# Kernel tuning notes

Measured on AMD Instinct MI355X. Metric: run time of the kernel, lower is better.

The kernel has to match this reference:

```python
import jax, jax.numpy as jnp
import numpy as np

HIDDEN = 1024
FRAME = 171
B = 128
T = 256


def _uniform(key, shape, fan):
    bound = 1.0 / np.sqrt(fan)
    return jax.random.uniform(key, shape, jnp.float32, -bound, bound)


def setup_inputs() -> dict:
    key = jax.random.key(0)
    ks = jax.random.split(key, 16)
    H, C = HIDDEN, FRAME
    inp = {
        "seq": jax.random.normal(ks[0], (B, T, C), jnp.float32),
        # LSTMCell 1 (input C -> H); torch layout: weight_ih [4H, in], weight_hh [4H, H]
        "w_ih1": _uniform(ks[1], (4 * H, C), H),
        "w_hh1": _uniform(ks[2], (4 * H, H), H),
        "b_ih1": _uniform(ks[3], (4 * H,), H),
        "b_hh1": _uniform(ks[4], (4 * H,), H),
        # LSTMCell 2 (H -> H)
        "w_ih2": _uniform(ks[5], (4 * H, H), H),
        "w_hh2": _uniform(ks[6], (4 * H, H), H),
        "b_ih2": _uniform(ks[7], (4 * H,), H),
        "b_hh2": _uniform(ks[8], (4 * H,), H),
        # LSTMCell 3 (H -> H)
        "w_ih3": _uniform(ks[9], (4 * H, H), H),
        "w_hh3": _uniform(ks[10], (4 * H, H), H),
        "b_ih3": _uniform(ks[11], (4 * H,), H),
        "b_hh3": _uniform(ks[12], (4 * H,), H),
        # Linear decoder H -> C
        "dec_w": _uniform(ks[13], (C, H), H),
        "dec_b": _uniform(ks[14], (C,), H),
        "gt": 5,
        "cond": 5,
    }
    return inp


def _lstm_cell(x, h, c, w_ih, w_hh, b_ih, b_hh):
    # torch.nn.LSTMCell: gates ordered (i, f, g, o)
    z = x @ w_ih.T + h @ w_hh.T + (b_ih + b_hh)  # [B, 4H]
    i, f, g, o = jnp.split(z, 4, axis=-1)
    c_new = jax.nn.sigmoid(f) * c + jax.nn.sigmoid(i) * jnp.tanh(g)
    h_new = jax.nn.sigmoid(o) * jnp.tanh(c_new)
    return h_new, c_new


def reference(seq, w_ih1, w_hh1, b_ih1, b_hh1,
              w_ih2, w_hh2, b_ih2, b_hh2,
              w_ih3, w_hh3, b_ih3, b_hh3,
              dec_w, dec_b, gt, cond):
    b, t, c = seq.shape
    h = seq.dtype
    # auto-conditioning pattern: gt ground-truth frames then cond self-fed frames
    pattern = (jnp.arange(t) % (gt + cond)) < gt  # [T] bool
    H = w_hh1.shape[1]
    zeros_h = jnp.zeros((b, H), h)
    init = (zeros_h, zeros_h, zeros_h, zeros_h, zeros_h, zeros_h,
            jnp.zeros((b, c), h))

    def step(carry, xs):
        h1, c1, h2, c2, h3, c3, xo = carry
        x_t, p_t = xs
        inp = jnp.where(p_t, x_t, xo)
        h1, c1 = _lstm_cell(inp, h1, c1, w_ih1, w_hh1, b_ih1, b_hh1)
        h2, c2 = _lstm_cell(h1, h2, c2, w_ih2, w_hh2, b_ih2, b_hh2)
        h3, c3 = _lstm_cell(h2, h3, c3, w_ih3, w_hh3, b_ih3, b_hh3)
        out = h3 @ dec_w.T + dec_b  # [B, C]
        return (h1, c1, h2, c2, h3, c3, out), out

    seq_t = jnp.transpose(seq, (1, 0, 2))  # [T, B, C]
    _, outs = jax.lax.scan(step, init, (seq_t, pattern))
    return jnp.transpose(outs, (1, 0, 2))  # [B, T, C]
```

## Files before the change

### kernel.cpp

```cpp
#include <hip/hip_runtime.h>
#include <math.h>

#define TSTEPS 256
#define CDIM 171
#define XSTR 6400
#define SEQB (TSTEPS*CDIM)

#define ARR_OFF   0
#define GF_OFF    2048
#define REL_OFF   2560
#define XCNT_OFF  3072
#define GREG_OFF  3080
#define ARR2_OFF  4096
#define NFLAGS    8192

typedef short v8s __attribute__((ext_vector_type(8)));
typedef float v4f __attribute__((ext_vector_type(4)));

static __device__ __forceinline__ unsigned short f2bf(float f) {
  unsigned int u = __float_as_uint(f);
  u += 0x7fffu + ((u >> 16) & 1u);
  return (unsigned short)(u >> 16);
}
static __device__ __forceinline__ float bf2f(unsigned short h) {
  return __uint_as_float(((unsigned int)h) << 16);
}
static __device__ __forceinline__ float sigf(float x) { return 1.0f / (1.0f + expf(-x)); }

static __device__ __forceinline__ bool probe_bf16(const unsigned int* w) {
  int c = 0;
  #pragma unroll
  for (int i = 0; i < 8; ++i) {
    unsigned e = (w[i] >> 7) & 0xFFu;
    c += (e >= 90u && e <= 145u) ? 1 : 0;
  }
  return c == 8;
}
static __device__ __forceinline__ float getv(const void* p, bool bf, size_t i) {
  return bf ? bf2f(((const unsigned short*)p)[i]) : ((const float*)p)[i];
}

static __device__ __forceinline__ unsigned ld_agent(const unsigned* p) {
  return __hip_atomic_load(p, __ATOMIC_RELAXED, __HIP_MEMORY_SCOPE_AGENT);
}
static __device__ __forceinline__ void st_agent(unsigned* p, unsigned v) {
  __hip_atomic_store(p, v, __ATOMIC_RELAXED, __HIP_MEMORY_SCOPE_AGENT);
}
static __device__ __forceinline__ void st_agent_us(unsigned short* p, unsigned short v) {
  __hip_atomic_store(p, v, __ATOMIC_RELAXED, __HIP_MEMORY_SCOPE_AGENT);
}

__global__ __launch_bounds__(256) void init_kernel(
    const void* seq, const void* wih1, const void* whh1,
    const void* bih1, const void* bhh1,
    const void* wih2, const void* whh2, const void* bih2, const void* bhh2,
    const void* wih3, const void* whh3, const void* bih3, const void* bhh3,
    const void* decw,
    unsigned short* __restrict__ X, float* __restrict__ BS,
    unsigned* __restrict__ flags,
    unsigned short* __restrict__ WL1, unsigned short* __restrict__ WL2,
    unsigned short* __restrict__ WL3, unsigned short* __restrict__ WDEC,
    unsigned short* __restrict__ XR, unsigned short* __restrict__ XGT,
    const int* __restrict__ gtp, const int* __restrict__ condp)
{
  const int tid = blockIdx.x * 256 + threadIdx.x;
  const int NT = 2048 * 256;
  const bool bfm = probe_bf16((const unsigned int*)seq);
  int gt = gtp[0];
  const bool p0 = 0 < gt;

  for (int i = tid; i < 128 * XSTR; i += NT) {
    int b = i / XSTR, c = i - b * XSTR;
    unsigned short v = 0;
    if (c < CDIM && p0) v = f2bf(getv(seq, bfm, (size_t)b * SEQB + c));
    X[i] = v;
  }
  for (int i = tid; i < 8 * 128 * XSTR; i += NT) {
    int r = i % (128 * XSTR);
    int b = r / XSTR, c = r - b * XSTR;
    unsigned short v = 0;
    if (c < CDIM && p0) v = f2bf(getv(seq, bfm, (size_t)b * SEQB + c));
    XR[i] = v;
  }
  const void* bis[3] = {bih1, bih2, bih3};
  const void* bhs[3] = {bhh1, bhh2, bhh3};
  for (int i = tid; i < 3 * 4096; i += NT) {
    int l = i >> 12, n = i & 4095;
    BS[i] = getv(bis[l], bfm, n) + getv(bhs[l], bfm, n);
  }
  for (int i = tid; i < NFLAGS; i += NT) flags[i] = 0u;
  for (int i = tid; i < 4096 * 1280; i += NT) {
    int r = i / 1280, c = i - r * 1280;
    float v;
    if (c < CDIM)      v = getv(wih1, bfm, (size_t)r * CDIM + c);
    else if (c < 256)  v = 0.f;
    else               v = getv(whh1, bfm, (size_t)r * 1024 + (c - 256));
    WL1[i] = f2bf(v);
  }
  for (int i = tid; i < 4096 * 2048; i += NT) {
    int r = i >> 11, c = i & 2047;
    size_t o = (size_t)r * 1024 + (c & 1023);
    WL2[i] = f2bf((c < 1024) ? getv(wih2, bfm, o) : getv(whh2, bfm, o));
    WL3[i] = f2bf((c < 1024) ? getv(wih3, bfm, o) : getv(whh3, bfm, o));
  }
  for (int i = tid; i < 176 * 1024; i += NT) {
    int r = i >> 10, c = i & 1023;
    WDEC[i] = (r < CDIM) ? f2bf(getv(decw, bfm, (size_t)r * 1024 + c)) : (unsigned short)0;
  }
  if (XGT) {
    for (int i = tid; i < TSTEPS * 128 * 256; i += NT) {
      int t = i >> 15, b = (i >> 8) & 127, c = i & 255;
      unsigned short v = 0;
      if (c < CDIM) v = f2bf(getv(seq, bfm, (size_t)b * SEQB + (size_t)t * CDIM + c));
      XGT[i] = v;
    }
  }
}

static __device__ __forceinline__ void gbar_nf(
    unsigned* fl, unsigned xcd, unsigned rank, unsigned NX, unsigned amask,
    unsigned G, int wave, int lane, unsigned& budget)
{
  __syncthreads();
  if (threadIdx.x == 0) st_agent(fl + ARR_OFF + xcd * 256 + rank, G);
  if (wave == 0) {
    if (rank == 0) {
      const unsigned* ab = fl + ARR_OFF + xcd * 256;
      for (;;) {
        unsigned ok = 1u;
        #pragma unroll
        for (int k = 0; k < 4; ++k) {
          unsigned r = (unsigned)lane + 64u * k;
          if (r < NX) ok &= (ld_agent(ab + r) >= G) ? 1u : 0u;
        }
        if (__all((int)ok)) break;
        if (budget == 0) break;
        --budget; __builtin_amdgcn_s_sleep(1);
      }
      st_agent(fl + GF_OFF + xcd * 64, G);
      for (;;) {
        unsigned ok = 1u;
        if (lane < 8 && ((amask >> lane) & 1u))
          ok = (ld_agent(fl + GF_OFF + (unsigned)lane * 64) >= G) ? 1u : 0u;
        if (__all((int)ok)) break;
        if (budget == 0) break;
        --budget; __builtin_amdgcn_s_sleep(1);
      }
      st_agent(fl + REL_OFF + xcd * 64, G);
    } else {
      unsigned* rp = fl + REL_OFF + xcd * 64;
      for (;;) {
        unsigned v = ld_agent(rp);
        if (__all((int)(v >= G))) break;
        if (budget == 0) break;
        --budget; __builtin_amdgcn_s_sleep(1);
      }
    }
  }
  __syncthreads();
}

static __device__ __forceinline__ void xcopy(
    unsigned short* __restrict__ dst, const unsigned short* __restrict__ src,
    int hoff, unsigned rank, unsigned NX, int tid)
{
  if (NX == 32u) {
    const unsigned d0 = rank * 256u + (unsigned)tid;
    unsigned vv[8];
    #pragma unroll
    for (int k = 0; k < 8; ++k) {
      unsigned d = d0 + 8192u * k;
      size_t off = (size_t)(d >> 9) * XSTR + hoff + ((size_t)(d & 511u) << 1);
      vv[k] = ld_agent((const unsigned*)(src + off));
    }
    #pragma unroll
    for (int k = 0; k < 8; ++k) {
      unsigned d = d0 + 8192u * k;
      size_t off = (size_t)(d >> 9) * XSTR + hoff + ((size_t)(d & 511u) << 1);
      *(unsigned*)(dst + off) = vv[k];
    }
  } else {
    for (unsigned d = rank * 256u + (unsigned)tid; d < 65536u; d += NX * 256u) {
      size_t off = (size_t)(d >> 9) * XSTR + hoff + ((size_t)(d & 511u) << 1);
      *(unsigned*)(dst + off) = ld_agent((const unsigned*)(src + off));
    }
  }
}

static __device__ __forceinline__ void xbar(
    unsigned* fl, unsigned xcd, unsigned rank, unsigned NX,
    unsigned G, int wave, int lane, unsigned& budget)
{
  __syncthreads();
  if (threadIdx.x == 0) st_agent(fl + ARR2_OFF + xcd * 256 + rank, G);
  if (wave == 0) {
    const unsigned* ab = fl + ARR2_OFF + xcd * 256;
    for (;;) {
      unsigned ok = 1u;
      #pragma unroll
      for (int k = 0; k < 4; ++k) {
        unsigned r = (unsigned)lane + 64u * k;
        if (r < NX) ok &= (ld_agent(ab + r) >= G) ? 1u : 0u;
      }
      if (__all((int)ok)) break;
      if (budget == 0) break;
      --budget; __builtin_amdgcn_s_sleep(1);
    }
    asm volatile("buffer_inv" ::: "memory");
  }
  __syncthreads();
}

template<int NCH>
static __device__ __forceinline__ void mfma_phase(
    const v8s* wf, const unsigned short* __restrict__ Xb,
    int a0, int bnd, int a1, int kbase, v4f* acc)
{
  #pragma unroll
  for (int i = 0; i < 8; ++i) acc[i] = (v4f){0.f, 0.f, 0.f, 0.f};
  #pragma unroll
  for (int c = 0; c < NCH; ++c) {
    const int acol = kbase + 32 * c;
    const int xcol = (acol < bnd) ? (a0 + acol) : (a1 + acol - bnd);
    const unsigned short* ap = Xb + xcol;
    #pragma unroll
    for (int m = 0; m < 8; ++m) {
      v8s a = *(const v8s*)(ap + (size_t)(16 * m) * XSTR);
      acc[m] = __builtin_amdgcn_mfma_f32_16x16x32_bf16(a, wf[c], acc[m], 0, 0, 0);
    }
  }
}

static __device__ __forceinline__ void lstm_epilogue(
    v4f* acc, float* lred, int wave, int lane,
    const float* bs4, float* cst2,
    unsigned short* __restrict__ X, int hoff, int g)
{
  const int l15 = lane & 15, quad = lane >> 4;
  float* myp = lred + wave * 2048;
  #pragma unroll
  for (int m = 0; m < 8; ++m)
    #pragma unroll
    for (int j = 0; j < 4; ++j)
      myp[m * 256 + l15 * 16 + ((4 * quad + j) ^ ((l15 >> 1) & 3))] = acc[m][j];
  __syncthreads();
  const int ri = lane >> 2, hc = lane & 3;
  #pragma unroll
  for (int e = 0; e < 2; ++e) {
    const int m = 2 * wave + e;
    float z[4];
    #pragma unroll
    for (int k = 0; k < 4; ++k) z[k] = bs4[k];
    #pragma unroll
    for (int w2 = 0; w2 < 4; ++w2) {
      const float* pp = lred + w2 * 2048 + m * 256;
      #pragma unroll
      for (int k = 0; k < 4; ++k) {
        const int col = hc + 4 * k;
        z[k] += pp[col * 16 + (ri ^ ((col >> 1) & 3))];
      }
    }
    float cn = sigf(z[1]) * cst2[e] + sigf(z[0]) * tanhf(z[2]);
    float h  = sigf(z[3]) * tanhf(cn);
    cst2[e] = cn;
    const int row = 32 * wave + 16 * e + ri;
    st_agent_us(X + (size_t)row * XSTR + hoff + 4 * g + hc, f2bf(h));
  }
}

static __device__ __forceinline__ void dec_tile(
    int dm2, int dn2, const unsigned short* __restrict__ WDEC,
    const unsigned short* __restrict__ XRb, int p_, float* lred,
    int wave, int lane, int l15, int quad,
    const void* __restrict__ decb, bool bf, bool wout, bool wx,
    void* __restrict__ outp, int t)
{
  v4f da = (v4f){0.f, 0.f, 0.f, 0.f};
  const unsigned short* wp = WDEC + (size_t)(16 * dn2 + l15) * 1024 + 256 * wave + 8 * quad;
  const unsigned short* ap = XRb + (size_t)(16 * dm2 + l15) * XSTR
                           + (4352 + 1024 * p_) + 256 * wave + 8 * quad;
  #pragma unroll
  for (int c = 0; c < 8; ++c) {
    v8s a = *(const v8s*)(ap + 32 * c);
    v8s w = *(const v8s*)(wp + 32 * c);
    da = __builtin_amdgcn_mfma_f32_16x16x32_bf16(a, w, da, 0, 0, 0);
  }
  float* myp = lred + wave * 2048;
  #pragma unroll
  for (int j = 0; j < 4; ++j)
    myp[l15 * 16 + ((4 * quad + j) ^ ((l15 >> 1) & 3))] = da[j];
  __syncthreads();
  if (wave == 0) {
    const int col = 16 * dn2 + l15;
    float dbv2 = (col < CDIM) ? getv(decb, bf, col) : 0.f;
    #pragma unroll
    for (int e = 0; e < 4; ++e) {
      const int r = 4 * e + quad;
      float v = dbv2;
      #pragma unroll
      for (int w2 = 0; w2 < 4; ++w2)
        v += lred[w2 * 2048 + l15 * 16 + (r ^ ((l15 >> 1) & 3))];
      if (col < CDIM) {
        const int brow = 16 * dm2 + r;
        if (wout) {
          const size_t oidx = (size_t)brow * SEQB + (size_t)t * CDIM + col;
          if (bf) ((unsigned short*)outp)[oidx] = f2bf(v);
          else    ((float*)outp)[oidx] = v;
        }
        if (wx) *(unsigned short*)((unsigned short*)XRb
                  + (size_t)brow * XSTR + col) = f2bf(v);
      }
    }
  }
  __syncthreads();
}

__global__ __launch_bounds__(256, 1) void persist(
    const unsigned short* __restrict__ WL1, const unsigned short* __restrict__ WL2,
    const unsigned short* __restrict__ WL3, const unsigned short* __restrict__ WDEC,
    const float* __restrict__ BS, unsigned short* __restrict__ X,
    unsigned* __restrict__ flags, unsigned short* __restrict__ XR,
    const void* __restrict__ seq, const void* __restrict__ decb,
    void* __restrict__ outp, const unsigned short* __restrict__ XGT,
    const int* __restrict__ gtp, const int* __restrict__ condp)
{
  const int g = blockIdx.x;
  const int tid = threadIdx.x, wave = tid >> 6, lane = tid & 63;
  const int l15 = lane & 15, quad = lane >> 4;
  const bool bf = probe_bf16((const unsigned int*)seq);
  int gt = gtp[0]; int per = gt + condp[0]; if (per < 1) per = 1;
  unsigned budget = 20000000u;

  __shared__ unsigned s_rank;
  unsigned xcd;
  asm volatile("s_getreg_b32 %0, hwreg(HW_REG_XCC_ID)" : "=s"(xcd));
  xcd &= 7u;
  if (tid == 0) {
    s_rank = __hip_atomic_fetch_add(flags + XCNT_OFF + xcd, 1u,
                                    __ATOMIC_RELAXED, __HIP_MEMORY_SCOPE_AGENT);
    __hip_atomic_fetch_add(flags + GREG_OFF, 1u,
                           __ATOMIC_RELEASE, __HIP_MEMORY_SCOPE_AGENT);
  }
  __syncthreads();
  const unsigned rank = s_rank;
  if (wave == 0 && lane == 0) {
    while (__hip_atomic_load(flags + GREG_OFF, __ATOMIC_ACQUIRE,
                             __HIP_MEMORY_SCOPE_AGENT) < 256u) {
      if (budget == 0) break;
      --budget; __builtin_amdgcn_s_sleep(4);
    }
  }
  __syncthreads();
  const unsigned NX = ld_agent(flags + XCNT_OFF + xcd);
  unsigned amask = 0;
  #pragma unroll
  for (int k = 0; k < 8; ++k)
    amask |= (ld_agent(flags + XCNT_OFF + k) > 0u ? 1u : 0u) << k;
  const unsigned owner = (unsigned)__builtin_ctz(amask | 0x100u);
  const bool isown = (xcd == owner);

  unsigned short* XRb = XR + (size_t)xcd * (128 * XSTR);

  const int br = 1024 * (l15 >> 2) + 4 * g + (l15 & 3);
  v8s w1f[10], w2f[16], w3f[16];
  {
    const unsigned short* p = WL1 + (size_t)br * 1280 + 320 * wave + 8 * quad;
    #pragma unroll
    for (int c = 0; c < 10; ++c) w1f[c] = *(const v8s*)(p + 32 * c);
  }
  {
    const unsigned short* p = WL2 + (size_t)br * 2048 + 512 * wave + 8 * quad;
    #pragma unroll
    for (int c = 0; c < 16; ++c) w2f[c] = *(const v8s*)(p + 32 * c);
  }
  {
    const unsigned short* p = WL3 + (size_t)br * 2048 + 512 * wave + 8 * quad;
    #pragma unroll
    for (int c = 0; c < 16; ++c) w3f[c] = *(const v8s*)(p + 32 * c);
  }
  const int dm = g / 11, dn = g - dm * 11;
  float bsr[3][4];
  #pragma unroll
  for (int l = 0; l < 3; ++l)
    #pragma unroll
    for (int gm = 0; gm < 4; ++gm)
      bsr[l][gm] = BS[4096 * l + 1024 * gm + 4 * g + (lane & 3)];

  float cst1[2] = {0.f, 0.f}, cst2v[2] = {0.f, 0.f}, cst3[2] = {0.f, 0.f};
  __shared__ float lred[8192];
  const unsigned short* Xb = XRb + (size_t)l15 * XSTR + 8 * quad;
  unsigned bgen = 0;
  v4f acc[8];

  for (int t = 0; t < TSTEPS; ++t) {
    const int p_ = t & 1, q_ = p_ ^ 1;
    const bool pt = (t % per) < gt;

    if (pt && wave == 0) {
      #pragma unroll
      for (int i = 0; i < 8; ++i) acc[i] = (v4f){0.f, 0.f, 0.f, 0.f};
      if (XGT) {
        const unsigned short* xb = XGT + ((size_t)t * 128 + l15) * 256 + 8 * quad;
        #pragma unroll
        for (int c = 0; c < 8; ++c) {
          #pragma unroll
          for (int m = 0; m < 8; ++m) {
            v8s a = *(const v8s*)(xb + 32 * c + (size_t)(16 * m) * 256);
            acc[m] = __builtin_amdgcn_mfma_f32_16x16x32_bf16(a, w1f[c], acc[m], 0, 0, 0);
          }
        }
      } else {
        #pragma unroll
        for (int c = 0; c < 8; ++c) {
          const int col0 = 32 * c + 8 * quad;
          #pragma unroll
          for (int m = 0; m < 8; ++m) {
            const size_t so = (size_t)(l15 + 16 * m) * SEQB + (size_t)t * CDIM;
            v8s a;
            #pragma unroll
            for (int j = 0; j < 8; ++j) {
              const int cc = col0 + j;
              unsigned short hv = 0;
              if (cc < CDIM)
                hv = bf ? ((const unsigned short*)seq)[so + cc]
                        : f2bf(((const float*)seq)[so + cc]);
              a[j] = (short)hv;
            }
            acc[m] = __builtin_amdgcn_mfma_f32_16x16x32_bf16(a, w1f[c], acc[m], 0, 0, 0);
          }
        }
      }
      #pragma unroll
      for (int c = 8; c < 10; ++c) {
        const unsigned short* ap = Xb + (256 + 1024 * q_) + (32 * c - 256);
        #pragma unroll
        for (int m = 0; m < 8; ++m) {
          v8s a = *(const v8s*)(ap + (size_t)(16 * m) * XSTR);
          acc[m] = __builtin_amdgcn_mfma_f32_16x16x32_bf16(a, w1f[c], acc[m], 0, 0, 0);
        }
      }
    } else {
      mfma_phase<10>(w1f, Xb, 0, 256, 256 + 1024 * q_, 320 * wave, acc);
    }
    lstm_epilogue(acc, lred, wave, lane, bsr[0], cst1, X, 256 + 1024 * p_, g);

    gbar_nf(flags, xcd, rank, NX, amask, ++bgen, wave, lane, budget);
    xcopy(XRb, X, 256 + 1024 * p_, rank, NX, tid);
    xbar(flags, xcd, rank, NX, bgen, wave, lane, budget);
    mfma_phase<16>(w2f, Xb, 256 + 1024 * p_, 1024, 2304 + 1024 * q_, 512 * wave, acc);
    lstm_epilogue(acc, lred, wave, lane, bsr[1], cst2v, X, 2304 + 1024 * p_, g);

    gbar_nf(flags, xcd, rank, NX, amask, ++bgen, wave, lane, budget);
    xcopy(XRb, X, 2304 + 1024 * p_, rank, NX, tid);
    xbar(flags, xcd, rank, NX, bgen, wave, lane, budget);
    mfma_phase<16>(w3f, Xb, 2304 + 1024 * p_, 1024, 4352 + 1024 * q_, 512 * wave, acc);
    lstm_epilogue(acc, lred, wave, lane, bsr[2], cst3, X, 4352 + 1024 * p_, g);

    gbar_nf(flags, xcd, rank, NX, amask, ++bgen, wave, lane, budget);
    xcopy(XRb, X, 4352 + 1024 * p_, rank, NX, tid);
    xbar(flags, xcd, rank, NX, bgen, wave, lane, budget);

    const bool pnext = ((t + 1) % per) < gt;
    const bool needx = (t < TSTEPS - 1) && !pnext;
    if (needx) {
      for (unsigned tt = rank; tt < 88u; tt += NX) {
        int dm2 = (int)(tt / 11u), dn2 = (int)(tt - (unsigned)dm2 * 11u);
        dec_tile(dm2, dn2, WDEC, XRb, p_, lred, wave, lane, l15, quad,
                 decb, bf, isown, true, outp, t);
      }
      ++bgen;
      xbar(flags, xcd, rank, NX, bgen, wave, lane, budget);
    } else if (g < 88) {
      dec_tile(dm, dn, WDEC, XRb, p_, lred, wave, lane, l15, quad,
               decb, bf, true, false, outp, t);
    }
  }
}

extern "C" void kernel_launch(void* const* d_in, const int* in_sizes, int n_in,
                              void* d_out, int out_size, void* d_ws, size_t ws_size,
                              hipStream_t stream) {
  const void* seq  = d_in[0];
  const void* wih1 = d_in[1];  const void* whh1 = d_in[2];
  const void* bih1 = d_in[3];  const void* bhh1 = d_in[4];
  const void* wih2 = d_in[5];  const void* whh2 = d_in[6];
  const void* bih2 = d_in[7];  const void* bhh2 = d_in[8];
  const void* wih3 = d_in[9];  const void* whh3 = d_in[10];
  const void* bih3 = d_in[11]; const void* bhh3 = d_in[12];
  const void* decw = d_in[13]; const void* decb = d_in[14];
  const int* gtp   = (const int*)d_in[15];
  const int* condp = (const int*)d_in[16];

  char* ws = (char*)d_ws;
  unsigned short* X    = (unsigned short*)(ws + 0);
  float*          BS   = (float*)(ws + 1638400);
  unsigned*       FLAGS= (unsigned*)(ws + 1687552);
  unsigned short* XR   = (unsigned short*)(ws + 1720320);
  unsigned short* WL1  = (unsigned short*)(ws + 14827520);
  unsigned short* WL2  = (unsigned short*)(ws + 25313280);
  unsigned short* WL3  = (unsigned short*)(ws + 42090496);
  unsigned short* WDEC = (unsigned short*)(ws + 58867712);
  unsigned short* XGT  = (ws_size >= (size_t)59228160 + (size_t)16777216)
                       ? (unsigned short*)(ws + 59228160) : (unsigned short*)0;

  init_kernel<<<2048, 256, 0, stream>>>(seq, wih1, whh1, bih1, bhh1,
                                        wih2, whh2, bih2, bhh2,
                                        wih3, whh3, bih3, bhh3, decw,
                                        X, BS, FLAGS, WL1, WL2, WL3, WDEC,
                                        XR, XGT, gtp, condp);

  persist<<<256, 256, 0, stream>>>(WL1, WL2, WL3, WDEC, BS, X, FLAGS, XR,
                                   seq, decb, d_out, XGT, gtp, condp);
}
```

Before: 16.06 ms.

## Defer decoder to next step with per-tile flags and flatten grid barrier

The decoder for step t now runs at the start of step t+1 on a single wave per tile, with no block-level reduction. Each tile publishes a per-tile flag, so layer 1 waits only on those flags when it needs the self-fed input, instead of a separate decode phase plus an extra barrier. The hierarchical per-XCD grid barrier is replaced by a flat barrier in which every block polls all 256 slots. Layer 1 also gets software-pipelined, cache-bypassing loads of the fed-back input. Together these aim to cut synchronisation and serial decode latency on the recurrent critical path, at the cost of more polling traffic and tighter memory-ordering assumptions.

```diff
diff --git a/kernel.cpp b/kernel.cpp
--- a/kernel.cpp
+++ b/kernel.cpp
@@ -6,13 +6,12 @@
 #define XSTR 6400
 #define SEQB (TSTEPS*CDIM)
 
-#define ARR_OFF   0
-#define GF_OFF    2048
-#define REL_OFF   2560
-#define XCNT_OFF  3072
-#define GREG_OFF  3080
-#define ARR2_OFF  4096
-#define NFLAGS    8192
+#define GB_OFF    0
+#define DECF_OFF  256
+#define XCNT_OFF  512
+#define GREG_OFF  520
+#define ARR2_OFF  1024
+#define NFLAGS    4096
 
 typedef short v8s __attribute__((ext_vector_type(8)));
 typedef float v4f __attribute__((ext_vector_type(4)));
@@ -48,6 +47,11 @@
 }
 static __device__ __forceinline__ void st_agent_us(unsigned short* p, unsigned short v) {
   __hip_atomic_store(p, v, __ATOMIC_RELAXED, __HIP_MEMORY_SCOPE_AGENT);
+}
+static __device__ __forceinline__ v8s lda16(const unsigned short* p) {
+  v8s v;
+  asm volatile("global_load_dwordx4 %0, %1, off sc1" : "=v"(v) : "v"(p));
+  return v;
 }
 
 __global__ __launch_bounds__(256) void init_kernel(
@@ -117,44 +121,20 @@
   }
 }
 
-static __device__ __forceinline__ void gbar_nf(
-    unsigned* fl, unsigned xcd, unsigned rank, unsigned NX, unsigned amask,
-    unsigned G, int wave, int lane, unsigned& budget)
-{
-  __syncthreads();
-  if (threadIdx.x == 0) st_agent(fl + ARR_OFF + xcd * 256 + rank, G);
+static __device__ __forceinline__ void gbar_flat(
+    unsigned* fl, int g, unsigned tgt, int wave, int lane, unsigned& budget)
+{
+  __syncthreads();
+  if (threadIdx.x == 0) st_agent(fl + GB_OFF + g, tgt);
   if (wave == 0) {
-    if (rank == 0) {
-      const unsigned* ab = fl + ARR_OFF + xcd * 256;
-      for (;;) {
-        unsigned ok = 1u;
-        #pragma unroll
-        for (int k = 0; k < 4; ++k) {
-          unsigned r = (unsigned)lane + 64u * k;
-          if (r < NX) ok &= (ld_agent(ab + r) >= G) ? 1u : 0u;
-        }
-        if (__all((int)ok)) break;
-        if (budget == 0) break;
-        --budget; __builtin_amdgcn_s_sleep(1);
-      }
-      st_agent(fl + GF_OFF + xcd * 64, G);
-      for (;;) {
-        unsigned ok = 1u;
-        if (lane < 8 && ((amask >> lane) & 1u))
-          ok = (ld_agent(fl + GF_OFF + (unsigned)lane * 64) >= G) ? 1u : 0u;
-        if (__all((int)ok)) break;
-        if (budget == 0) break;
-        --budget; __builtin_amdgcn_s_sleep(1);
-      }
-      st_agent(fl + REL_OFF + xcd * 64, G);
-    } else {
-      unsigned* rp = fl + REL_OFF + xcd * 64;
-      for (;;) {
-        unsigned v = ld_agent(rp);
-        if (__all((int)(v >= G))) break;
-        if (budget == 0) break;
-        --budget; __builtin_amdgcn_s_sleep(1);
-      }
+    const unsigned* b = fl + GB_OFF;
+    for (;;) {
+      unsigned a0 = ld_agent(b + lane),       a1 = ld_agent(b + 64 + lane);
+      unsigned a2 = ld_agent(b + 128 + lane), a3 = ld_agent(b + 192 + lane);
+      if (__all((int)((a0 >= tgt) & (a1 >= tgt) & (a2 >= tgt) & (a3 >= tgt))))
+        break;
+      if (budget == 0) break;
+      --budget; __builtin_amdgcn_s_sleep(1);
     }
   }
   __syncthreads();
@@ -194,6 +174,7 @@
   __syncthreads();
   if (threadIdx.x == 0) st_agent(fl + ARR2_OFF + xcd * 256 + rank, G);
   if (wave == 0) {
+    asm volatile("buffer_inv" ::: "memory");
     const unsigned* ab = fl + ARR2_OFF + xcd * 256;
     for (;;) {
       unsigned ok = 1u;
@@ -206,7 +187,6 @@
       if (budget == 0) break;
       --budget; __builtin_amdgcn_s_sleep(1);
     }
-    asm volatile("buffer_inv" ::: "memory");
   }
   __syncthreads();
 }
@@ -266,53 +246,6 @@
     const int row = 32 * wave + 16 * e + ri;
     st_agent_us(X + (size_t)row * XSTR + hoff + 4 * g + hc, f2bf(h));
   }
-}
-
-static __device__ __forceinline__ void dec_tile(
-    int dm2, int dn2, const unsigned short* __restrict__ WDEC,
-    const unsigned short* __restrict__ XRb, int p_, float* lred,
-    int wave, int lane, int l15, int quad,
-    const void* __restrict__ decb, bool bf, bool wout, bool wx,
-    void* __restrict__ outp, int t)
-{
-  v4f da = (v4f){0.f, 0.f, 0.f, 0.f};
-  const unsigned short* wp = WDEC + (size_t)(16 * dn2 + l15) * 1024 + 256 * wave + 8 * quad;
-  const unsigned short* ap = XRb + (size_t)(16 * dm2 + l15) * XSTR
-                           + (4352 + 1024 * p_) + 256 * wave + 8 * quad;
-  #pragma unroll
-  for (int c = 0; c < 8; ++c) {
-    v8s a = *(const v8s*)(ap + 32 * c);
-    v8s w = *(const v8s*)(wp + 32 * c);
-    da = __builtin_amdgcn_mfma_f32_16x16x32_bf16(a, w, da, 0, 0, 0);
-  }
-  float* myp = lred + wave * 2048;
-  #pragma unroll
-  for (int j = 0; j < 4; ++j)
-    myp[l15 * 16 + ((4 * quad + j) ^ ((l15 >> 1) & 3))] = da[j];
-  __syncthreads();
-  if (wave == 0) {
-    const int col = 16 * dn2 + l15;
-    float dbv2 = (col < CDIM) ? getv(decb, bf, col) : 0.f;
-    #pragma unroll
-    for (int e = 0; e < 4; ++e) {
-      const int r = 4 * e + quad;
-      float v = dbv2;
-      #pragma unroll
-      for (int w2 = 0; w2 < 4; ++w2)
-        v += lred[w2 * 2048 + l15 * 16 + (r ^ ((l15 >> 1) & 3))];
-      if (col < CDIM) {
-        const int brow = 16 * dm2 + r;
-        if (wout) {
-          const size_t oidx = (size_t)brow * SEQB + (size_t)t * CDIM + col;
-          if (bf) ((unsigned short*)outp)[oidx] = f2bf(v);
-          else    ((float*)outp)[oidx] = v;
-        }
-        if (wx) *(unsigned short*)((unsigned short*)XRb
-                  + (size_t)brow * XSTR + col) = f2bf(v);
-      }
-    }
-  }
-  __syncthreads();
 }
 
 __global__ __launch_bounds__(256, 1) void persist(
@@ -352,12 +285,6 @@
   }
   __syncthreads();
   const unsigned NX = ld_agent(flags + XCNT_OFF + xcd);
-  unsigned amask = 0;
-  #pragma unroll
-  for (int k = 0; k < 8; ++k)
-    amask |= (ld_agent(flags + XCNT_OFF + k) > 0u ? 1u : 0u) << k;
-  const unsigned owner = (unsigned)__builtin_ctz(amask | 0x100u);
-  const bool isown = (xcd == owner);
 
   unsigned short* XRb = XR + (size_t)xcd * (128 * XSTR);
 
@@ -385,50 +312,121 @@
     #pragma unroll
     for (int gm = 0; gm < 4; ++gm)
       bsr[l][gm] = BS[4096 * l + 1024 * gm + 4 * g + (lane & 3)];
+  float dbv = 0.f;
+  if (g < 88) { int col = 16 * dn + l15; if (col < CDIM) dbv = getv(decb, bf, col); }
 
   float cst1[2] = {0.f, 0.f}, cst2v[2] = {0.f, 0.f}, cst3[2] = {0.f, 0.f};
   __shared__ float lred[8192];
   const unsigned short* Xb = XRb + (size_t)l15 * XSTR + 8 * quad;
-  unsigned bgen = 0;
+  unsigned bgen = 0, dg = 0;
   v4f acc[8];
 
   for (int t = 0; t < TSTEPS; ++t) {
     const int p_ = t & 1, q_ = p_ ^ 1;
     const bool pt = (t % per) < gt;
-
-    if (pt && wave == 0) {
+    if (t > 0 && !pt) ++dg;
+
+    if (t > 0 && wave == 0 && g < 88) {
+      const unsigned short* ap = XRb + (size_t)(16 * dm + l15) * XSTR
+                               + (4352 + 1024 * q_) + 8 * quad;
+      const unsigned short* wp = WDEC + (size_t)(16 * dn + l15) * 1024 + 8 * quad;
+      v4f da = (v4f){0.f, 0.f, 0.f, 0.f};
+      #pragma unroll
+      for (int c = 0; c < 32; ++c) {
+        v8s a = *(const v8s*)(ap + 32 * c);
+        v8s w = *(const v8s*)(wp + 32 * c);
+        da = __builtin_amdgcn_mfma_f32_16x16x32_bf16(a, w, da, 0, 0, 0);
+      }
+      const int col = 16 * dn + l15;
+      #pragma unroll
+      for (int j = 0; j < 4; ++j) {
+        float v = da[j] + dbv;
+        const int brow = 16 * dm + 4 * quad + j;
+        if (col < CDIM) {
+          const size_t oidx = (size_t)brow * SEQB + (size_t)(t - 1) * CDIM + col;
+          if (bf) ((unsigned short*)outp)[oidx] = f2bf(v);
+          else    ((float*)outp)[oidx] = v;
+          if (!pt) st_agent_us(X + (size_t)brow * XSTR + col, f2bf(v));
+        }
+      }
+      if (!pt) {
+        asm volatile("s_waitcnt vmcnt(0)" ::: "memory");
+        if (lane == 0) st_agent(flags + DECF_OFF + g, dg);
+      }
+    }
+
+    if (wave == 0) {
       #pragma unroll
       for (int i = 0; i < 8; ++i) acc[i] = (v4f){0.f, 0.f, 0.f, 0.f};
-      if (XGT) {
-        const unsigned short* xb = XGT + ((size_t)t * 128 + l15) * 256 + 8 * quad;
-        #pragma unroll
-        for (int c = 0; c < 8; ++c) {
+      if (pt) {
+        if (XGT) {
+          const unsigned short* xb = XGT + ((size_t)t * 128 + l15) * 256 + 8 * quad;
           #pragma unroll
-          for (int m = 0; m < 8; ++m) {
-            v8s a = *(const v8s*)(xb + 32 * c + (size_t)(16 * m) * 256);
-            acc[m] = __builtin_amdgcn_mfma_f32_16x16x32_bf16(a, w1f[c], acc[m], 0, 0, 0);
+          for (int c = 0; c < 8; ++c)
+            #pragma unroll
+            for (int m = 0; m < 8; ++m) {
+              v8s a = *(const v8s*)(xb + 32 * c + (size_t)(16 * m) * 256);
+              acc[m] = __builtin_amdgcn_mfma_f32_16x16x32_bf16(a, w1f[c], acc[m], 0, 0, 0);
+            }
+        } else {
+          #pragma unroll
+          for (int c = 0; c < 8; ++c) {
+            const int col0 = 32 * c + 8 * quad;
+            #pragma unroll
+            for (int m = 0; m < 8; ++m) {
+              const size_t so = (size_t)(l15 + 16 * m) * SEQB + (size_t)t * CDIM;
+              v8s a;
+              #pragma unroll
+              for (int j = 0; j < 8; ++j) {
+                const int cc = col0 + j;
+                unsigned short hv = 0;
+                if (cc < CDIM)
+                  hv = bf ? ((const unsigned short*)seq)[so + cc]
+                          : f2bf(((const float*)seq)[so + cc]);
+                a[j] = (short)hv;
+              }
+              acc[m] = __builtin_amdgcn_mfma_f32_16x16x32_bf16(a, w1f[c], acc[m], 0, 0, 0);
+            }
           }
         }
       } else {
-        #pragma unroll
-        for (int c = 0; c < 8; ++c) {
-          const int col0 = 32 * c + 8 * quad;
-          #pragma unroll
-          for (int m = 0; m < 8; ++m) {
-            const size_t so = (size_t)(l15 + 16 * m) * SEQB + (size_t)t * CDIM;
-            v8s a;
-            #pragma unroll
-            for (int j = 0; j < 8; ++j) {
-              const int cc = col0 + j;
-              unsigned short hv = 0;
-              if (cc < CDIM)
-                hv = bf ? ((const unsigned short*)seq)[so + cc]
-                        : f2bf(((const float*)seq)[so + cc]);
-              a[j] = (short)hv;
-            }
-            acc[m] = __builtin_amdgcn_mfma_f32_16x16x32_bf16(a, w1f[c], acc[m], 0, 0, 0);
+        if (t > 0) {
+          const unsigned* df = flags + DECF_OFF;
+          for (;;) {
+            unsigned a = ld_agent(df + lane);
+            unsigned b2 = (lane < 24) ? ld_agent(df + 64 + lane) : dg;
+            if (__all((int)((a >= dg) & (b2 >= dg)))) break;
+            if (budget == 0) break;
+            --budget; __builtin_amdgcn_s_sleep(1);
           }
         }
+        v8s bA[8], bB[8];
+        #define XISSUE(BUF, MM) do { \
+            const unsigned short* bp_ = X + (size_t)(l15 + 16 * (MM)) * XSTR + 8 * quad; \
+            _Pragma("unroll") \
+            for (int c_ = 0; c_ < 8; ++c_) BUF[c_] = lda16(bp_ + 32 * c_); \
+          } while (0)
+        XISSUE(bA, 0);
+        #pragma unroll
+        for (int mm = 0; mm < 8; mm += 2) {
+          XISSUE(bB, mm + 1);
+          asm volatile("s_waitcnt vmcnt(8)" ::: "memory");
+          __builtin_amdgcn_sched_barrier(0);
+          #pragma unroll
+          for (int c = 0; c < 8; ++c)
+            acc[mm] = __builtin_amdgcn_mfma_f32_16x16x32_bf16(bA[c], w1f[c], acc[mm], 0, 0, 0);
+          if (mm + 2 < 8) {
+            XISSUE(bA, mm + 2);
+            asm volatile("s_waitcnt vmcnt(8)" ::: "memory");
+          } else {
+            asm volatile("s_waitcnt vmcnt(0)" ::: "memory");
+          }
+          __builtin_amdgcn_sched_barrier(0);
+          #pragma unroll
+          for (int c = 0; c < 8; ++c)
+            acc[mm + 1] = __builtin_amdgcn_mfma_f32_16x16x32_bf16(bB[c], w1f[c], acc[mm + 1], 0, 0, 0);
+        }
+        #undef XISSUE
       }
       #pragma unroll
       for (int c = 8; c < 10; ++c) {
@@ -444,35 +442,44 @@
     }
     lstm_epilogue(acc, lred, wave, lane, bsr[0], cst1, X, 256 + 1024 * p_, g);
 
-    gbar_nf(flags, xcd, rank, NX, amask, ++bgen, wave, lane, budget);
+    gbar_flat(flags, g, ++bgen, wave, lane, budget);
     xcopy(XRb, X, 256 + 1024 * p_, rank, NX, tid);
     xbar(flags, xcd, rank, NX, bgen, wave, lane, budget);
     mfma_phase<16>(w2f, Xb, 256 + 1024 * p_, 1024, 2304 + 1024 * q_, 512 * wave, acc);
     lstm_epilogue(acc, lred, wave, lane, bsr[1], cst2v, X, 2304 + 1024 * p_, g);
 
-    gbar_nf(flags, xcd, rank, NX, amask, ++bgen, wave, lane, budget);
+    gbar_flat(flags, g, ++bgen, wave, lane, budget);
     xcopy(XRb, X, 2304 + 1024 * p_, rank, NX, tid);
     xbar(flags, xcd, rank, NX, bgen, wave, lane, budget);
     mfma_phase<16>(w3f, Xb, 2304 + 1024 * p_, 1024, 4352 + 1024 * q_, 512 * wave, acc);
     lstm_epilogue(acc, lred, wave, lane, bsr[2], cst3, X, 4352 + 1024 * p_, g);
 
-    gbar_nf(flags, xcd, rank, NX, amask, ++bgen, wave, lane, budget);
+    gbar_flat(flags, g, ++bgen, wave, lane, budget);
     xcopy(XRb, X, 4352 + 1024 * p_, rank, NX, tid);
     xbar(flags, xcd, rank, NX, bgen, wave, lane, budget);
-
-    const bool pnext = ((t + 1) % per) < gt;
-    const bool needx = (t < TSTEPS - 1) && !pnext;
-    if (needx) {
-      for (unsigned tt = rank; tt < 88u; tt += NX) {
-        int dm2 = (int)(tt / 11u), dn2 = (int)(tt - (unsigned)dm2 * 11u);
-        dec_tile(dm2, dn2, WDEC, XRb, p_, lred, wave, lane, l15, quad,
-                 decb, bf, isown, true, outp, t);
-      }
-      ++bgen;
-      xbar(flags, xcd, rank, NX, bgen, wave, lane, budget);
-    } else if (g < 88) {
-      dec_tile(dm, dn, WDEC, XRb, p_, lred, wave, lane, l15, quad,
-               decb, bf, true, false, outp, t);
+  }
+
+  if (wave == 0 && g < 88) {
+    const unsigned short* ap = XRb + (size_t)(16 * dm + l15) * XSTR
+                             + (4352 + 1024 * 1) + 8 * quad;
+    const unsigned short* wp = WDEC + (size_t)(16 * dn + l15) * 1024 + 8 * quad;
+    v4f da = (v4f){0.f, 0.f, 0.f, 0.f};
+    #pragma unroll
+    for (int c = 0; c < 32; ++c) {
+      v8s a = *(const v8s*)(ap + 32 * c);
+      v8s w = *(const v8s*)(wp + 32 * c);
+      da = __builtin_amdgcn_mfma_f32_16x16x32_bf16(a, w, da, 0, 0, 0);
+    }
+    const int col = 16 * dn + l15;
+    #pragma unroll
+    for (int j = 0; j < 4; ++j) {
+      float v = da[j] + dbv;
+      const int brow = 16 * dm + 4 * quad + j;
+      if (col < CDIM) {
+        const size_t oidx = (size_t)brow * SEQB + (size_t)255 * CDIM + col;
+        if (bf) ((unsigned short*)outp)[oidx] = f2bf(v);
+        else    ((float*)outp)[oidx] = v;
+      }
     }
   }
 }
```

Measured after the change: 17.19 ms. 7.1% more time.
